# Kernel tuning notes

Hardware: AMD Instinct MI355X
Metric: run time of the kernel (lower is better)

Reference implementation:

```python
import jax, jax.numpy as jnp
import numpy as np

# ---- module config (init kwargs) ----
EMB = 256
HIDDEN = 256
L, H, P = 4, 8, 4
CH = HIDDEN // H
PADDING_MODE = "zeros"   # 'zeros' or 'border'
ALIGN_CORNERS = False
# feature pyramid level shapes (height, width), static
SHAPES = np.array([[128, 128], [64, 64], [32, 32], [16, 16]], dtype=np.int32)
LEVEL_STARTS = np.concatenate([[0], np.cumsum(SHAPES.prod(-1))[:-1]]).astype(np.int32)

B, N = 8, 1024
I = int(SHAPES.prod(-1).sum())  # 21760


def setup_inputs() -> dict:
    key = jax.random.key(0)
    ks = jax.random.split(key, 8)
    scale = 0.02
    return {
        "img": jax.random.normal(ks[0], (B, I, EMB), jnp.float32),
        "img_shapes": jnp.asarray(SHAPES),
        "queries": jax.random.normal(ks[1], (B, N, EMB), jnp.float32),
        "reference_points": jax.random.uniform(ks[2], (B, N, 2), dtype=jnp.float32),
        "W_img": jax.random.normal(ks[3], (EMB, HIDDEN), jnp.float32) * scale,
        "b_img": jnp.zeros((HIDDEN,), jnp.float32),
        "W_q": jax.random.normal(ks[4], (EMB, H * L * P * 3), jnp.float32) * scale,
        "b_q": jnp.zeros((H * L * P * 3,), jnp.float32),
        "W_out": jax.random.normal(ks[5], (HIDDEN, EMB), jnp.float32) * scale,
        "b_out": jnp.zeros((EMB,), jnp.float32),
    }


def _msda(img, points, attn):
    """Multiscale deformable attention core.
    img:    [B, I, H, CH] flattened pyramid features
    points: [B, N, H, L, P, 2] (x, y) in [0, 1]
    attn:   [B, N, H, L, P]
    returns [B, N, H, CH]
    """
    b, _, h_, ch = img.shape
    n = points.shape[1]
    img_t = img.transpose(0, 2, 1, 3)  # [B, H, I, CH]
    levels = []
    for l in range(L):
        hh, ww = int(SHAPES[l, 0]), int(SHAPES[l, 1])
        start = int(LEVEL_STARTS[l])
        p = points[:, :, :, l]  # [B, N, H, P, 2]
        # grid_sample pixel mapping (after the module's 2*p-1 normalization)
        if ALIGN_CORNERS:
            x = p[..., 0] * (ww - 1)
            y = p[..., 1] * (hh - 1)
        else:
            x = p[..., 0] * ww - 0.5
            y = p[..., 1] * hh - 0.5
        x0 = jnp.floor(x); y0 = jnp.floor(y)
        wx = x - x0;       wy = y - y0
        x0i = x0.astype(jnp.int32); y0i = y0.astype(jnp.int32)
        acc = jnp.zeros((b, h_, n * P, ch), img.dtype)
        corners = [
            (x0i,     y0i,     (1 - wx) * (1 - wy)),
            (x0i + 1, y0i,     wx * (1 - wy)),
            (x0i,     y0i + 1, (1 - wx) * wy),
            (x0i + 1, y0i + 1, wx * wy),
        ]
        for xi, yi, cw in corners:
            if PADDING_MODE == "zeros":
                valid = (xi >= 0) & (xi < ww) & (yi >= 0) & (yi < hh)
                cw = cw * valid.astype(cw.dtype)
            xc = jnp.clip(xi, 0, ww - 1)
            yc = jnp.clip(yi, 0, hh - 1)
            idx = start + yc * ww + xc                              # [B, N, H, P]
            idx_t = idx.transpose(0, 2, 1, 3).reshape(b, h_, n * P)  # [B, H, N*P]
            g = jnp.take_along_axis(img_t, idx_t[..., None], axis=2)  # [B, H, N*P, CH]
            cw_t = cw.transpose(0, 2, 1, 3).reshape(b, h_, n * P, 1)
            acc = acc + cw_t * g
        levels.append(acc.reshape(b, h_, n, P, ch))
    samples = jnp.stack(levels, axis=3)            # [B, H, N, L, P, CH]
    attn_t = attn.transpose(0, 2, 1, 3, 4)          # [B, H, N, L, P]
    return jnp.einsum("bhnlpc,bhnlp->bnhc", samples, attn_t)


def reference(img, img_shapes, queries, reference_points, W_img, b_img, W_q, b_q, W_out, b_out):
    b, i_, _ = img.shape
    n = queries.shape[1]
    qp = (queries @ W_q + b_q).reshape(b, n, H, L, P, 3)
    offsets = qp[..., :2]                            # [B, N, H, L, P, 2]
    attn = jax.nn.softmax(qp[..., 2].reshape(b, n, H, L * P), axis=-1).reshape(b, n, H, L, P)
    img_p = (img @ W_img + b_img).reshape(b, i_, H, CH)
    shapes_f = img_shapes.astype(jnp.float32)        # [L, 2] (h, w)
    # faithful to source: offsets / img_shapes[:, None, :]
    sampling_points = reference_points[:, :, None, None, None, :] + offsets / shapes_f[:, None, :]
    out = _msda(img_p, sampling_points, attn)        # [B, N, H, CH]
    return out.reshape(b, n, HIDDEN) @ W_out + b_out
```

## Files before the change

kernel.cpp:

```cpp
#include <hip/hip_runtime.h>
#include <type_traits>
#include <utility>

#define B_    8
#define NQ_   1024
#define I_    21760
#define EMB_  256
#define HID_  256
#define H_    8
#define CH_   32

typedef float  f32x4  __attribute__((ext_vector_type(4)));
typedef __bf16 bf16x8 __attribute__((ext_vector_type(8)));
typedef short  s16x8  __attribute__((ext_vector_type(8)));

template <typename V, typename = void>
struct bf16_mfma_native : std::false_type {};
template <typename V>
struct bf16_mfma_native<V, std::void_t<decltype(__builtin_amdgcn_mfma_f32_16x16x32_bf16(
    std::declval<V>(), std::declval<V>(), std::declval<f32x4>(), 0, 0, 0))>>
    : std::true_type {};

template <typename V>
__device__ __forceinline__ f32x4 mfma_dispatch(V a, V b, f32x4 c) {
  if constexpr (bf16_mfma_native<V>::value) {
    return __builtin_amdgcn_mfma_f32_16x16x32_bf16(a, b, c, 0, 0, 0);
  } else {
    return __builtin_amdgcn_mfma_f32_16x16x32_bf16(
        __builtin_bit_cast(s16x8, a), __builtin_bit_cast(s16x8, b), c, 0, 0, 0);
  }
}

__device__ __forceinline__ f32x4 MFMA(s16x8 a, s16x8 b, f32x4 c) {
  return mfma_dispatch(__builtin_bit_cast(bf16x8, a), __builtin_bit_cast(bf16x8, b), c);
}

__device__ __forceinline__ unsigned short f2bf(float f) {
  unsigned u = __float_as_uint(f);
  u += 0x7fffu + ((u >> 16) & 1u);
  return (unsigned short)(u >> 16);
}

template <int NS, bool OUT_BF16>
__global__ __launch_bounds__(512) void gemm_k256(
    const float* __restrict__ A, const float* __restrict__ W,
    const float* __restrict__ bias, void* __restrict__ Out,
    const int N, const int Mtiles) {
  __shared__ __align__(16) short lds[32 * 264];
  const int tid  = threadIdx.x;
  const int lane = tid & 63;
  const int wave = tid >> 6;
  const int quad = lane >> 4;
  const int ln   = lane & 15;

  s16x8 bfrag[NS][8];
  float bv[NS];
#pragma unroll
  for (int st = 0; st < NS; ++st) {
    const int ng = st * 128 + wave * 16 + ln;
    bv[st] = bias[ng];
#pragma unroll
    for (int ks = 0; ks < 8; ++ks) {
      s16x8 f;
#pragma unroll
      for (int j = 0; j < 8; ++j)
        f[j] = (short)f2bf(W[(ks * 32 + quad * 8 + j) * N + ng]);
      bfrag[st][ks] = f;
    }
  }

  const int sr = tid >> 4;
  const int sc = (tid & 15) * 16;

  for (int t = blockIdx.x; t < Mtiles; t += gridDim.x) {
    const size_t rowBase = (size_t)t * 32;
    {
      const float4* src = (const float4*)(A + (rowBase + sr) * 256 + sc);
      float4 v0 = src[0], v1 = src[1], v2 = src[2], v3 = src[3];
      s16x8 p0, p1;
      p0[0] = (short)f2bf(v0.x); p0[1] = (short)f2bf(v0.y);
      p0[2] = (short)f2bf(v0.z); p0[3] = (short)f2bf(v0.w);
      p0[4] = (short)f2bf(v1.x); p0[5] = (short)f2bf(v1.y);
      p0[6] = (short)f2bf(v1.z); p0[7] = (short)f2bf(v1.w);
      p1[0] = (short)f2bf(v2.x); p1[1] = (short)f2bf(v2.y);
      p1[2] = (short)f2bf(v2.z); p1[3] = (short)f2bf(v2.w);
      p1[4] = (short)f2bf(v3.x); p1[5] = (short)f2bf(v3.y);
      p1[6] = (short)f2bf(v3.z); p1[7] = (short)f2bf(v3.w);
      *(s16x8*)&lds[sr * 264 + sc]     = p0;
      *(s16x8*)&lds[sr * 264 + sc + 8] = p1;
    }
    __syncthreads();

    f32x4 acc[NS][2];
#pragma unroll
    for (int st = 0; st < NS; ++st) {
      acc[st][0] = f32x4{bv[st], bv[st], bv[st], bv[st]};
      acc[st][1] = acc[st][0];
    }
#pragma unroll
    for (int ks = 0; ks < 8; ++ks) {
      s16x8 a0 = *(const s16x8*)&lds[ln * 264 + ks * 32 + quad * 8];
      s16x8 a1 = *(const s16x8*)&lds[(ln + 16) * 264 + ks * 32 + quad * 8];
#pragma unroll
      for (int st = 0; st < NS; ++st) {
        acc[st][0] = MFMA(a0, bfrag[st][ks], acc[st][0]);
        acc[st][1] = MFMA(a1, bfrag[st][ks], acc[st][1]);
      }
    }
#pragma unroll
    for (int st = 0; st < NS; ++st) {
      const int ng = st * 128 + wave * 16 + ln;
#pragma unroll
      for (int rt = 0; rt < 2; ++rt) {
#pragma unroll
        for (int r = 0; r < 4; ++r) {
          const size_t m = rowBase + rt * 16 + quad * 4 + r;
          if constexpr (OUT_BF16)
            ((unsigned short*)Out)[m * N + ng] = f2bf(acc[st][rt][r]);
          else
            ((float*)Out)[m * N + ng] = acc[st][rt][r];
        }
      }
    }
    __syncthreads();
  }
}

__global__ __launch_bounds__(512) void qproj_softmax_kernel(
    const float* __restrict__ A, const float* __restrict__ W,
    const float* __restrict__ bias, const float* __restrict__ refp,
    float* __restrict__ attn, float* __restrict__ pts) {
  constexpr int N = 384;
  __shared__ __align__(16) char smem[32 * 392 * 4];
  short* slds = (short*)smem;
  float* sout = (float*)smem;
  const int tid  = threadIdx.x;
  const int lane = tid & 63;
  const int wave = tid >> 6;
  const int quad = lane >> 4;
  const int ln   = lane & 15;

  s16x8 bfrag[3][8];
  float bv[3];
#pragma unroll
  for (int st = 0; st < 3; ++st) {
    const int ng = st * 128 + wave * 16 + ln;
    bv[st] = bias[ng];
#pragma unroll
    for (int ks = 0; ks < 8; ++ks) {
      s16x8 f;
#pragma unroll
      for (int j = 0; j < 8; ++j)
        f[j] = (short)f2bf(W[(ks * 32 + quad * 8 + j) * N + ng]);
      bfrag[st][ks] = f;
    }
  }

  const int sr = tid >> 4;
  const int sc = (tid & 15) * 16;
  const size_t rowBase = (size_t)blockIdx.x * 32;
  {
    const float4* src = (const float4*)(A + (rowBase + sr) * 256 + sc);
    float4 v0 = src[0], v1 = src[1], v2 = src[2], v3 = src[3];
    s16x8 p0, p1;
    p0[0] = (short)f2bf(v0.x); p0[1] = (short)f2bf(v0.y);
    p0[2] = (short)f2bf(v0.z); p0[3] = (short)f2bf(v0.w);
    p0[4] = (short)f2bf(v1.x); p0[5] = (short)f2bf(v1.y);
    p0[6] = (short)f2bf(v1.z); p0[7] = (short)f2bf(v1.w);
    p1[0] = (short)f2bf(v2.x); p1[1] = (short)f2bf(v2.y);
    p1[2] = (short)f2bf(v2.z); p1[3] = (short)f2bf(v2.w);
    p1[4] = (short)f2bf(v3.x); p1[5] = (short)f2bf(v3.y);
    p1[6] = (short)f2bf(v3.z); p1[7] = (short)f2bf(v3.w);
    *(s16x8*)&slds[sr * 264 + sc]     = p0;
    *(s16x8*)&slds[sr * 264 + sc + 8] = p1;
  }
  __syncthreads();

  f32x4 acc[3][2];
#pragma unroll
  for (int st = 0; st < 3; ++st) {
    acc[st][0] = f32x4{bv[st], bv[st], bv[st], bv[st]};
    acc[st][1] = acc[st][0];
  }
#pragma unroll
  for (int ks = 0; ks < 8; ++ks) {
    s16x8 a0 = *(const s16x8*)&slds[ln * 264 + ks * 32 + quad * 8];
    s16x8 a1 = *(const s16x8*)&slds[(ln + 16) * 264 + ks * 32 + quad * 8];
#pragma unroll
    for (int st = 0; st < 3; ++st) {
      acc[st][0] = MFMA(a0, bfrag[st][ks], acc[st][0]);
      acc[st][1] = MFMA(a1, bfrag[st][ks], acc[st][1]);
    }
  }
  __syncthreads();

#pragma unroll
  for (int st = 0; st < 3; ++st) {
    const int ng = st * 128 + wave * 16 + ln;
#pragma unroll
    for (int rt = 0; rt < 2; ++rt)
#pragma unroll
      for (int r = 0; r < 4; ++r)
        sout[(rt * 16 + quad * 4 + r) * 392 + ng] = acc[st][rt][r];
  }
  __syncthreads();

  if (tid < 256) {
    const int ql = tid >> 3, h = tid & 7;
    const float* basep = sout + ql * 392 + h * 48;
    float s[16];
    float mx = -1e30f;
#pragma unroll
    for (int lp = 0; lp < 16; ++lp) {
      s[lp] = basep[lp * 3 + 2];
      mx = fmaxf(mx, s[lp]);
    }
    float sum = 0.f;
#pragma unroll
    for (int lp = 0; lp < 16; ++lp) {
      s[lp] = __expf(s[lp] - mx);
      sum += s[lp];
    }
    const float inv = 1.0f / sum;
    const size_t q   = rowBase + ql;
    const size_t gq8 = q * 8 + h;
    float* ao = attn + gq8 * 16;
#pragma unroll
    for (int lp = 0; lp < 16; ++lp) ao[lp] = s[lp] * inv;

    const float rx = refp[q * 2], ry = refp[q * 2 + 1];
    float* po = pts + gq8 * 32;
    const float invsh[4] = {1.f / 128.f, 1.f / 64.f, 1.f / 32.f, 1.f / 16.f};
#pragma unroll
    for (int l = 0; l < 4; ++l) {
#pragma unroll
      for (int p = 0; p < 4; ++p) {
        const int lp = l * 4 + p;
        po[lp * 2 + 0] = rx + basep[lp * 3 + 0] * invsh[l];
        po[lp * 2 + 1] = ry + basep[lp * 3 + 1] * invsh[l];
      }
    }
  }
}

__global__ __launch_bounds__(256) void msda_sample_kernel(
    const unsigned int* __restrict__ imgp,
    const float* __restrict__ attn, const float* __restrict__ pts,
    float* __restrict__ out) {
  __shared__ __align__(16) float sw[512][4];
  __shared__ __align__(16) int   sib[512][4];
  const int bid = blockIdx.x;
  const int tid = threadIdx.x;

#pragma unroll
  for (int it = 0; it < 2; ++it) {
    const int i  = it * 256 + tid;
    const int q  = i >> 7;
    const int h  = (i >> 4) & 7;
    const int lp = i & 15;
    const int l  = lp >> 2;
    const int gq = bid * 4 + q;
    const int b  = gq >> 10;
    const int ww = 128 >> l;
    const int start = (l > 0 ? 16384 : 0) + (l > 1 ? 4096 : 0) + (l > 2 ? 1024 : 0);
    const float2 p = *(const float2*)&pts[((size_t)gq * 8 + h) * 32 + lp * 2];
    const float a  = attn[((size_t)gq * 8 + h) * 16 + lp];
    const float x = p.x * (float)ww - 0.5f;
    const float y = p.y * (float)ww - 0.5f;
    const float x0f = floorf(x), y0f = floorf(y);
    const float wx = x - x0f, wy = y - y0f;
    const int x0 = (int)x0f, y0 = (int)y0f;
    const float cw[4] = {(1.f - wx) * (1.f - wy), wx * (1.f - wy),
                         (1.f - wx) * wy,          wx * wy};
#pragma unroll
    for (int c = 0; c < 4; ++c) {
      const int xi = x0 + (c & 1), yi = y0 + (c >> 1);
      const bool valid = (xi >= 0) & (xi < ww) & (yi >= 0) & (yi < ww);
      const int xc = min(max(xi, 0), ww - 1);
      const int yc = min(max(yi, 0), ww - 1);
      const int idx = start + yc * ww + xc;
      sw[i][c]  = valid ? a * cw[c] : 0.f;
      sib[i][c] = ((b * I_ + idx) << 7) + (h << 4);
    }
  }
  __syncthreads();

  const int q  = tid >> 6;
  const int h  = (tid >> 3) & 7;
  const int c4 = tid & 7;
  float a0 = 0.f, a1 = 0.f, a2 = 0.f, a3 = 0.f;
#pragma unroll
  for (int lp = 0; lp < 16; ++lp) {
    const int sidx = q * 128 + h * 16 + lp;
    const float4 w4 = *(const float4*)sw[sidx];
    const int4   i4 = *(const int4*)sib[sidx];
    uint2 u;
#define CORNER(IDX, WGT)                                  \
    u = *(const uint2*)&imgp[(IDX) + c4 * 2];             \
    a0 += (WGT) * __uint_as_float(u.x << 16);             \
    a1 += (WGT) * __uint_as_float(u.x & 0xffff0000u);     \
    a2 += (WGT) * __uint_as_float(u.y << 16);             \
    a3 += (WGT) * __uint_as_float(u.y & 0xffff0000u);
    CORNER(i4.x, w4.x)
    CORNER(i4.y, w4.y)
    CORNER(i4.z, w4.z)
    CORNER(i4.w, w4.w)
#undef CORNER
  }
  const int gq = bid * 4 + q;
  float4 r{a0, a1, a2, a3};
  *(float4*)&out[(size_t)gq * 256 + h * 32 + c4 * 4] = r;
}

#define OFF_IMGP 0ULL
#define OFF_ATTN 89128960ULL
#define OFF_PTS  93323264ULL
#define OFF_MSDA 101711872ULL
#define WS_NEEDED 110100480ULL

extern "C" void kernel_launch(void* const* d_in, const int* in_sizes, int n_in,
                              void* d_out, int out_size, void* d_ws, size_t ws_size,
                              hipStream_t stream) {
  const float* img     = (const float*)d_in[0];
  const float* queries = (const float*)d_in[2];
  const float* refp    = (const float*)d_in[3];
  const float* W_img   = (const float*)d_in[4];
  const float* b_img   = (const float*)d_in[5];
  const float* W_q     = (const float*)d_in[6];
  const float* b_q     = (const float*)d_in[7];
  const float* W_out   = (const float*)d_in[8];
  const float* b_out   = (const float*)d_in[9];

  if (ws_size < WS_NEEDED) return;

  char* ws = (char*)d_ws;
  unsigned short* imgp = (unsigned short*)(ws + OFF_IMGP);
  float* attn = (float*)(ws + OFF_ATTN);
  float* pts  = (float*)(ws + OFF_PTS);
  float* msda = (float*)(ws + OFF_MSDA);

  hipLaunchKernelGGL((gemm_k256<2, true>), dim3(544), dim3(512), 0, stream,
                     img, W_img, b_img, (void*)imgp, 256, I_ * B_ / 32);
  hipLaunchKernelGGL(qproj_softmax_kernel, dim3(B_ * NQ_ / 32), dim3(512), 0, stream,
                     queries, W_q, b_q, refp, attn, pts);
  hipLaunchKernelGGL(msda_sample_kernel, dim3(B_ * NQ_ / 4), dim3(256), 0, stream,
                     (const unsigned int*)imgp, attn, pts, msda);
  hipLaunchKernelGGL((gemm_k256<2, false>), dim3(256), dim3(512), 0, stream,
                     msda, W_out, b_out, d_out, 256, B_ * NQ_ / 32);
}
```

Before: 359.7 us.

## Double-buffer 64-row GEMM tiles and widen MSDA gathers to 16-byte loads

The projection GEMM moves from 32-row to 64-row tiles in a persistent loop with two LDS buffers. The next tile's global loads are issued before the current tile's MFMAs, and the operands are swapped so each lane writes contiguous vectorised outputs. The sampling kernel now covers 8 queries per block and has each thread gather 8 bf16 channels with uint4 loads instead of 4, and the q-proj staging load is made coalesced. The costs are higher register and LDS pressure, fewer blocks in the grid, and fewer threads per corner gather.

Result: faster. 340.6 us (-5.3%).

```diff
diff --git a/kernel.cpp b/kernel.cpp
--- a/kernel.cpp
+++ b/kernel.cpp
@@ -41,24 +41,26 @@
   return (unsigned short)(u >> 16);
 }
 
-template <int NS, bool OUT_BF16>
-__global__ __launch_bounds__(512) void gemm_k256(
+template <bool OUT_BF16>
+__global__ __launch_bounds__(512, 2) void gemm64(
     const float* __restrict__ A, const float* __restrict__ W,
     const float* __restrict__ bias, void* __restrict__ Out,
-    const int N, const int Mtiles) {
-  __shared__ __align__(16) short lds[32 * 264];
+    const int Mtiles) {
+  constexpr int N = 256;
+  constexpr int LDSTRIDE = 272;
+  __shared__ __align__(16) short lds[2][64 * LDSTRIDE];
   const int tid  = threadIdx.x;
   const int lane = tid & 63;
   const int wave = tid >> 6;
   const int quad = lane >> 4;
   const int ln   = lane & 15;
 
-  s16x8 bfrag[NS][8];
-  float bv[NS];
-#pragma unroll
-  for (int st = 0; st < NS; ++st) {
+  s16x8 bfrag[2][8];
+  f32x4 bias4[2];
+#pragma unroll
+  for (int st = 0; st < 2; ++st) {
     const int ng = st * 128 + wave * 16 + ln;
-    bv[st] = bias[ng];
+    bias4[st] = *(const f32x4*)&bias[st * 128 + wave * 16 + quad * 4];
 #pragma unroll
     for (int ks = 0; ks < 8; ++ks) {
       s16x8 f;
@@ -69,64 +71,90 @@
     }
   }
 
-  const int sr = tid >> 4;
-  const int sc = (tid & 15) * 16;
-
-  for (int t = blockIdx.x; t < Mtiles; t += gridDim.x) {
-    const size_t rowBase = (size_t)t * 32;
-    {
-      const float4* src = (const float4*)(A + (rowBase + sr) * 256 + sc);
-      float4 v0 = src[0], v1 = src[1], v2 = src[2], v3 = src[3];
-      s16x8 p0, p1;
-      p0[0] = (short)f2bf(v0.x); p0[1] = (short)f2bf(v0.y);
-      p0[2] = (short)f2bf(v0.z); p0[3] = (short)f2bf(v0.w);
-      p0[4] = (short)f2bf(v1.x); p0[5] = (short)f2bf(v1.y);
-      p0[6] = (short)f2bf(v1.z); p0[7] = (short)f2bf(v1.w);
-      p1[0] = (short)f2bf(v2.x); p1[1] = (short)f2bf(v2.y);
-      p1[2] = (short)f2bf(v2.z); p1[3] = (short)f2bf(v2.w);
-      p1[4] = (short)f2bf(v3.x); p1[5] = (short)f2bf(v3.y);
-      p1[6] = (short)f2bf(v3.z); p1[7] = (short)f2bf(v3.w);
-      *(s16x8*)&lds[sr * 264 + sc]     = p0;
-      *(s16x8*)&lds[sr * 264 + sc + 8] = p1;
-    }
-    __syncthreads();
-
-    f32x4 acc[NS][2];
-#pragma unroll
-    for (int st = 0; st < NS; ++st) {
-      acc[st][0] = f32x4{bv[st], bv[st], bv[st], bv[st]};
-      acc[st][1] = acc[st][0];
-    }
+  const int srow0 = wave * 8;
+
+  float4 pf[8];
+  int t = blockIdx.x;
+  {
+    const float* Ab = A + (size_t)t * 64 * 256;
+#pragma unroll
+    for (int j = 0; j < 8; ++j) pf[j] = ((const float4*)Ab)[j * 512 + tid];
+#pragma unroll
+    for (int j = 0; j < 8; ++j) {
+      const int row = j * 8 + wave;
+      uint2 u;
+      u.x = (unsigned)f2bf(pf[j].x) | ((unsigned)f2bf(pf[j].y) << 16);
+      u.y = (unsigned)f2bf(pf[j].z) | ((unsigned)f2bf(pf[j].w) << 16);
+      *(uint2*)&lds[0][row * LDSTRIDE + lane * 4] = u;
+    }
+  }
+  __syncthreads();
+  (void)srow0;
+
+  int p = 0;
+  while (t < Mtiles) {
+    const int tn = t + gridDim.x;
+    const bool more = (tn < Mtiles);
+    if (more) {
+      const float* Ab = A + (size_t)tn * 64 * 256;
+#pragma unroll
+      for (int j = 0; j < 8; ++j) pf[j] = ((const float4*)Ab)[j * 512 + tid];
+    }
+
+    f32x4 acc[2][4];
+#pragma unroll
+    for (int st = 0; st < 2; ++st)
+#pragma unroll
+      for (int rt = 0; rt < 4; ++rt) acc[st][rt] = bias4[st];
+
 #pragma unroll
     for (int ks = 0; ks < 8; ++ks) {
-      s16x8 a0 = *(const s16x8*)&lds[ln * 264 + ks * 32 + quad * 8];
-      s16x8 a1 = *(const s16x8*)&lds[(ln + 16) * 264 + ks * 32 + quad * 8];
-#pragma unroll
-      for (int st = 0; st < NS; ++st) {
-        acc[st][0] = MFMA(a0, bfrag[st][ks], acc[st][0]);
-        acc[st][1] = MFMA(a1, bfrag[st][ks], acc[st][1]);
-      }
-    }
-#pragma unroll
-    for (int st = 0; st < NS; ++st) {
-      const int ng = st * 128 + wave * 16 + ln;
-#pragma unroll
-      for (int rt = 0; rt < 2; ++rt) {
-#pragma unroll
-        for (int r = 0; r < 4; ++r) {
-          const size_t m = rowBase + rt * 16 + quad * 4 + r;
-          if constexpr (OUT_BF16)
-            ((unsigned short*)Out)[m * N + ng] = f2bf(acc[st][rt][r]);
-          else
-            ((float*)Out)[m * N + ng] = acc[st][rt][r];
+      s16x8 a[4];
+#pragma unroll
+      for (int rt = 0; rt < 4; ++rt)
+        a[rt] = *(const s16x8*)&lds[p][(rt * 16 + ln) * LDSTRIDE + ks * 32 + quad * 8];
+#pragma unroll
+      for (int st = 0; st < 2; ++st)
+#pragma unroll
+        for (int rt = 0; rt < 4; ++rt)
+          acc[st][rt] = MFMA(bfrag[st][ks], a[rt], acc[st][rt]);
+    }
+
+    const size_t rowBase = (size_t)t * 64;
+#pragma unroll
+    for (int st = 0; st < 2; ++st) {
+      const int col = st * 128 + wave * 16 + quad * 4;
+#pragma unroll
+      for (int rt = 0; rt < 4; ++rt) {
+        const size_t row = rowBase + rt * 16 + ln;
+        if constexpr (OUT_BF16) {
+          uint2 u;
+          u.x = (unsigned)f2bf(acc[st][rt][0]) | ((unsigned)f2bf(acc[st][rt][1]) << 16);
+          u.y = (unsigned)f2bf(acc[st][rt][2]) | ((unsigned)f2bf(acc[st][rt][3]) << 16);
+          *(uint2*)&((unsigned short*)Out)[row * N + col] = u;
+        } else {
+          *(f32x4*)&((float*)Out)[row * N + col] = acc[st][rt];
         }
       }
     }
-    __syncthreads();
-  }
-}
-
-__global__ __launch_bounds__(512) void qproj_softmax_kernel(
+
+    if (more) {
+#pragma unroll
+      for (int j = 0; j < 8; ++j) {
+        const int row = j * 8 + wave;
+        uint2 u;
+        u.x = (unsigned)f2bf(pf[j].x) | ((unsigned)f2bf(pf[j].y) << 16);
+        u.y = (unsigned)f2bf(pf[j].z) | ((unsigned)f2bf(pf[j].w) << 16);
+        *(uint2*)&lds[p ^ 1][row * LDSTRIDE + lane * 4] = u;
+      }
+      __syncthreads();
+    }
+    p ^= 1;
+    t = tn;
+  }
+}
+
+__global__ __launch_bounds__(512, 2) void qproj_softmax_kernel(
     const float* __restrict__ A, const float* __restrict__ W,
     const float* __restrict__ bias, const float* __restrict__ refp,
     float* __restrict__ attn, float* __restrict__ pts) {
@@ -156,23 +184,18 @@
     }
   }
 
-  const int sr = tid >> 4;
-  const int sc = (tid & 15) * 16;
   const size_t rowBase = (size_t)blockIdx.x * 32;
   {
-    const float4* src = (const float4*)(A + (rowBase + sr) * 256 + sc);
-    float4 v0 = src[0], v1 = src[1], v2 = src[2], v3 = src[3];
-    s16x8 p0, p1;
-    p0[0] = (short)f2bf(v0.x); p0[1] = (short)f2bf(v0.y);
-    p0[2] = (short)f2bf(v0.z); p0[3] = (short)f2bf(v0.w);
-    p0[4] = (short)f2bf(v1.x); p0[5] = (short)f2bf(v1.y);
-    p0[6] = (short)f2bf(v1.z); p0[7] = (short)f2bf(v1.w);
-    p1[0] = (short)f2bf(v2.x); p1[1] = (short)f2bf(v2.y);
-    p1[2] = (short)f2bf(v2.z); p1[3] = (short)f2bf(v2.w);
-    p1[4] = (short)f2bf(v3.x); p1[5] = (short)f2bf(v3.y);
-    p1[6] = (short)f2bf(v3.z); p1[7] = (short)f2bf(v3.w);
-    *(s16x8*)&slds[sr * 264 + sc]     = p0;
-    *(s16x8*)&slds[sr * 264 + sc + 8] = p1;
+    const float* Ab = A + rowBase * 256;
+#pragma unroll
+    for (int j = 0; j < 4; ++j) {
+      float4 v = ((const float4*)Ab)[j * 512 + tid];
+      const int row = j * 8 + wave;
+      uint2 u;
+      u.x = (unsigned)f2bf(v.x) | ((unsigned)f2bf(v.y) << 16);
+      u.y = (unsigned)f2bf(v.z) | ((unsigned)f2bf(v.w) << 16);
+      *(uint2*)&slds[row * 264 + lane * 4] = u;
+    }
   }
   __syncthreads();
 
@@ -247,19 +270,19 @@
     const unsigned int* __restrict__ imgp,
     const float* __restrict__ attn, const float* __restrict__ pts,
     float* __restrict__ out) {
-  __shared__ __align__(16) float sw[512][4];
-  __shared__ __align__(16) int   sib[512][4];
+  __shared__ __align__(16) float sw[1024][4];
+  __shared__ __align__(16) int   sib[1024][4];
   const int bid = blockIdx.x;
   const int tid = threadIdx.x;
 
 #pragma unroll
-  for (int it = 0; it < 2; ++it) {
+  for (int it = 0; it < 4; ++it) {
     const int i  = it * 256 + tid;
     const int q  = i >> 7;
     const int h  = (i >> 4) & 7;
     const int lp = i & 15;
     const int l  = lp >> 2;
-    const int gq = bid * 4 + q;
+    const int gq = bid * 8 + q;
     const int b  = gq >> 10;
     const int ww = 128 >> l;
     const int start = (l > 0 ? 16384 : 0) + (l > 1 ? 4096 : 0) + (l > 2 ? 1024 : 0);
@@ -285,31 +308,44 @@
   }
   __syncthreads();
 
-  const int q  = tid >> 6;
-  const int h  = (tid >> 3) & 7;
-  const int c4 = tid & 7;
-  float a0 = 0.f, a1 = 0.f, a2 = 0.f, a3 = 0.f;
+  const int q  = tid >> 5;
+  const int h  = (tid >> 2) & 7;
+  const int c8 = tid & 3;
+  float2 acc[4];
+#pragma unroll
+  for (int k = 0; k < 4; ++k) acc[k] = float2{0.f, 0.f};
+
+#define BFLO(v) __uint_as_float((v) << 16)
+#define BFHI(v) __uint_as_float((v) & 0xffff0000u)
 #pragma unroll
   for (int lp = 0; lp < 16; ++lp) {
     const int sidx = q * 128 + h * 16 + lp;
     const float4 w4 = *(const float4*)sw[sidx];
     const int4   i4 = *(const int4*)sib[sidx];
-    uint2 u;
-#define CORNER(IDX, WGT)                                  \
-    u = *(const uint2*)&imgp[(IDX) + c4 * 2];             \
-    a0 += (WGT) * __uint_as_float(u.x << 16);             \
-    a1 += (WGT) * __uint_as_float(u.x & 0xffff0000u);     \
-    a2 += (WGT) * __uint_as_float(u.y << 16);             \
-    a3 += (WGT) * __uint_as_float(u.y & 0xffff0000u);
-    CORNER(i4.x, w4.x)
-    CORNER(i4.y, w4.y)
-    CORNER(i4.z, w4.z)
-    CORNER(i4.w, w4.w)
-#undef CORNER
-  }
-  const int gq = bid * 4 + q;
-  float4 r{a0, a1, a2, a3};
-  *(float4*)&out[(size_t)gq * 256 + h * 32 + c4 * 4] = r;
+    const uint4 u0 = *(const uint4*)&imgp[i4.x + c8 * 4];
+    const uint4 u1 = *(const uint4*)&imgp[i4.y + c8 * 4];
+    const uint4 u2 = *(const uint4*)&imgp[i4.z + c8 * 4];
+    const uint4 u3 = *(const uint4*)&imgp[i4.w + c8 * 4];
+#define ACCUM(U, WGT)                                        \
+    acc[0].x += (WGT) * BFLO(U.x); acc[0].y += (WGT) * BFHI(U.x); \
+    acc[1].x += (WGT) * BFLO(U.y); acc[1].y += (WGT) * BFHI(U.y); \
+    acc[2].x += (WGT) * BFLO(U.z); acc[2].y += (WGT) * BFHI(U.z); \
+    acc[3].x += (WGT) * BFLO(U.w); acc[3].y += (WGT) * BFHI(U.w);
+    ACCUM(u0, w4.x)
+    ACCUM(u1, w4.y)
+    ACCUM(u2, w4.z)
+    ACCUM(u3, w4.w)
+#undef ACCUM
+  }
+#undef BFLO
+#undef BFHI
+
+  const int gq = bid * 8 + q;
+  float* dst = &out[(size_t)gq * 256 + h * 32 + c8 * 8];
+  float4 r0{acc[0].x, acc[0].y, acc[1].x, acc[1].y};
+  float4 r1{acc[2].x, acc[2].y, acc[3].x, acc[3].y};
+  *(float4*)dst = r0;
+  *(float4*)(dst + 4) = r1;
 }
 
 #define OFF_IMGP 0ULL
@@ -339,12 +375,12 @@
   float* pts  = (float*)(ws + OFF_PTS);
   float* msda = (float*)(ws + OFF_MSDA);
 
-  hipLaunchKernelGGL((gemm_k256<2, true>), dim3(544), dim3(512), 0, stream,
-                     img, W_img, b_img, (void*)imgp, 256, I_ * B_ / 32);
+  hipLaunchKernelGGL((gemm64<true>), dim3(256), dim3(512), 0, stream,
+                     img, W_img, b_img, (void*)imgp, I_ * B_ / 64);
   hipLaunchKernelGGL(qproj_softmax_kernel, dim3(B_ * NQ_ / 32), dim3(512), 0, stream,
                      queries, W_q, b_q, refp, attn, pts);
-  hipLaunchKernelGGL(msda_sample_kernel, dim3(B_ * NQ_ / 4), dim3(256), 0, stream,
+  hipLaunchKernelGGL(msda_sample_kernel, dim3(B_ * NQ_ / 8), dim3(256), 0, stream,
                      (const unsigned int*)imgp, attn, pts, msda);
-  hipLaunchKernelGGL((gemm_k256<2, false>), dim3(256), dim3(512), 0, stream,
-                     msda, W_out, b_out, d_out, 256, B_ * NQ_ / 32);
-}
+  hipLaunchKernelGGL((gemm64<false>), dim3(128), dim3(512), 0, stream,
+                     msda, W_out, b_out, d_out, 128);
+}
```
